# Performance work log

Hardware: AMD Instinct MI355X
Metric: run time of the kernel (lower is better)

## Reference

```python
import jax, jax.numpy as jnp
import numpy as np
from jax import lax

K = 8          # neighbors
LOSS_NORM = 2  # Lp norm over coords


def setup_inputs() -> dict:
    key = jax.random.key(0)
    k1, k2, k3 = jax.random.split(key, 3)
    B, N = 4, 8192
    return {
        "pc_source": jax.random.normal(k1, (B, N, 3), dtype=jnp.float32),
        "pc_target": jax.random.normal(k2, (B, N, 3), dtype=jnp.float32),
        "pred_flow": jax.random.normal(k3, (B, N, 3), dtype=jnp.float32),
    }


def _knn_idx(query, points, k):
    # query: [B,N,3], points: [B,M,3] -> idx [B,N,k] of k nearest points per query
    # squared euclidean pairwise distances (ranking-equivalent to euclidean)
    q2 = jnp.sum(query * query, axis=-1, keepdims=True)          # [B,N,1]
    p2 = jnp.sum(points * points, axis=-1)[:, None, :]           # [B,1,M]
    d2 = q2 + p2 - 2.0 * jnp.einsum("bnd,bmd->bnm", query, points)  # [B,N,M]
    _, idx = lax.top_k(-d2, k)                                   # smallest-k
    return idx


def _gather_points(points, idx):
    # points: [B,M,3], idx: [B,N,k] -> [B,N,k,3]
    return jax.vmap(lambda p, i: p[i])(points, idx)


def reference(pc_source, pc_target, pred_flow):
    pc_pred = pc_source + pred_flow                               # [B,N,3]

    # knn indices are detached in the original (idx.detach())
    idx1 = _knn_idx(lax.stop_gradient(pc_pred), lax.stop_gradient(pc_target), K)
    nn1 = _gather_points(pc_target, idx1)                         # [B,N,K,3]
    diff1 = pc_pred[:, :, None, :] - nn1                          # [B,N,K,3]
    dist1 = jnp.linalg.norm(diff1, ord=LOSS_NORM, axis=-1).mean(axis=-1)  # [B,N]

    idx2 = _knn_idx(lax.stop_gradient(pc_target), lax.stop_gradient(pc_pred), K)
    nn2 = _gather_points(pc_pred, idx2)                           # [B,M,K,3]
    diff2 = pc_target[:, :, None, :] - nn2
    dist2 = jnp.linalg.norm(diff2, ord=LOSS_NORM, axis=-1).mean(axis=-1)  # [B,M]

    return (dist1 + dist2).mean()
```

## Files before the change

### kernel.cpp

```cpp
#include <hip/hip_runtime.h>
#include <math.h>

constexpr int B = 4;
constexpr int N = 8192;
constexpr int KNN = 8;
constexpr int NCELL = 4096;
constexpr int GSIZE = 16;
constexpr int NGRP = N / GSIZE;
constexpr int QPB = 64;
constexpr int WAVES = 8;
constexpr int NCB = 2 * B;

__device__ __forceinline__ void insert8(float (&d)[KNN], float tv) {
  float n0 = fminf(d[0], tv);
  float n1 = __builtin_amdgcn_fmed3f(d[0], d[1], tv);
  float n2 = __builtin_amdgcn_fmed3f(d[1], d[2], tv);
  float n3 = __builtin_amdgcn_fmed3f(d[2], d[3], tv);
  float n4 = __builtin_amdgcn_fmed3f(d[3], d[4], tv);
  float n5 = __builtin_amdgcn_fmed3f(d[4], d[5], tv);
  float n6 = __builtin_amdgcn_fmed3f(d[5], d[6], tv);
  float n7 = __builtin_amdgcn_fmed3f(d[6], d[7], tv);
  d[0] = n0; d[1] = n1; d[2] = n2; d[3] = n3;
  d[4] = n4; d[5] = n5; d[6] = n6; d[7] = n7;
}

__device__ __forceinline__ int morton3(int x, int y, int z) {
  int m = 0;
#pragma unroll
  for (int b = 0; b < 4; ++b)
    m |= (((x >> b) & 1) << (3 * b + 2)) | (((y >> b) & 1) << (3 * b + 1)) |
         (((z >> b) & 1) << (3 * b + 0));
  return m;
}

__device__ __forceinline__ int point_cell(float x, float y, float z) {
  int cx = (int)fminf(fmaxf((x + 4.0f) * 2.0f, 0.0f), 15.0f);
  int cy = (int)fminf(fmaxf((y + 4.0f) * 2.0f, 0.0f), 15.0f);
  int cz = (int)fminf(fmaxf((z + 4.0f) * 2.0f, 0.0f), 15.0f);
  return morton3(cx, cy, cz);
}

__global__ __launch_bounds__(1024) void prep_kernel(
    const float* __restrict__ src, const float* __restrict__ tgt,
    const float* __restrict__ flow, float4* __restrict__ pred_s,
    float4* __restrict__ tgt_s, int* __restrict__ starts,
    float4* __restrict__ gbox, float* __restrict__ out) {
  __shared__ int hist[NCELL];
  __shared__ int wsum[16];
  int tid = threadIdx.x, cb = blockIdx.x;
  int cloud = cb >> 2, batch = cb & 3;
  if (cb == 0 && tid == 0) out[0] = 0.0f;

  for (int i = tid; i < NCELL; i += 1024) hist[i] = 0;
  __syncthreads();

  const float* __restrict__ bp = (cloud == 0 ? src : tgt) + batch * N * 3;
  const float* __restrict__ bf = flow + batch * N * 3;
  float4 pt[8];
  int cell[8];
#pragma unroll
  for (int k = 0; k < 8; ++k) {
    int i = k * 1024 + tid;
    float x = bp[3 * i + 0], y = bp[3 * i + 1], z = bp[3 * i + 2];
    if (cloud == 0) { x += bf[3 * i + 0]; y += bf[3 * i + 1]; z += bf[3 * i + 2]; }
    pt[k] = make_float4(x, y, z, 0.5f * (x * x + y * y + z * z));
    cell[k] = point_cell(x, y, z);
    atomicAdd(&hist[cell[k]], 1);
  }
  __syncthreads();

  int b4 = tid * 4;
  int h0v = hist[b4 + 0], h1v = hist[b4 + 1];
  int h2v = hist[b4 + 2], h3v = hist[b4 + 3];
  int s = h0v + h1v + h2v + h3v;
  int lane = tid & 63, w = tid >> 6;
  int incl = s;
#pragma unroll
  for (int off = 1; off < 64; off <<= 1) {
    int u = __shfl_up(incl, off, 64);
    if (lane >= off) incl += u;
  }
  if (lane == 63) wsum[w] = incl;
  __syncthreads();
  if (tid < 16) {
    int v = wsum[tid], inc = v;
#pragma unroll
    for (int off = 1; off < 16; off <<= 1) {
      int u = __shfl_up(inc, off, 64);
      if (tid >= off) inc += u;
    }
    wsum[tid] = inc - v;
  }
  __syncthreads();
  int run = incl - s + wsum[w];
  int* __restrict__ stg = starts + cb * (NCELL + 1);
  stg[b4 + 0] = run; hist[b4 + 0] = run; run += h0v;
  stg[b4 + 1] = run; hist[b4 + 1] = run; run += h1v;
  stg[b4 + 2] = run; hist[b4 + 2] = run; run += h2v;
  stg[b4 + 3] = run; hist[b4 + 3] = run; run += h3v;
  if (tid == 0) stg[NCELL] = N;
  __syncthreads();

  float4* __restrict__ dst = (cloud == 0 ? pred_s : tgt_s) + batch * N;
#pragma unroll
  for (int k = 0; k < 8; ++k) {
    int pos = atomicAdd(&hist[cell[k]], 1);
    dst[pos] = pt[k];
  }
  __threadfence_block();
  __syncthreads();

  if (tid < NGRP) {
    const float4* __restrict__ sp = dst + tid * GSIZE;
    float lx = INFINITY, ly = INFINITY, lz = INFINITY;
    float hx = -INFINITY, hy = -INFINITY, hz = -INFINITY;
#pragma unroll
    for (int t = 0; t < GSIZE; ++t) {
      float4 p = sp[t];
      lx = fminf(lx, p.x); ly = fminf(ly, p.y); lz = fminf(lz, p.z);
      hx = fmaxf(hx, p.x); hy = fmaxf(hy, p.y); hz = fmaxf(hz, p.z);
    }
    gbox[cb * 2 * NGRP + 2 * tid + 0] = make_float4(lx, ly, lz, 0.0f);
    gbox[cb * 2 * NGRP + 2 * tid + 1] = make_float4(hx, hy, hz, 0.0f);
  }
}

__global__ __launch_bounds__(512, 8) void chamfer_kernel(
    const float4* __restrict__ pred_s, const float4* __restrict__ tgt_s,
    const float4* __restrict__ aabb, float* __restrict__ out) {
  int blk = blockIdx.x;
  int dir = blk >> 9;
  int batch = (blk >> 7) & 3;
  int chunk = blk & 127;
  const float4* __restrict__ qarr = (dir == 0 ? pred_s : tgt_s) + batch * N;
  const float4* __restrict__ parr = (dir == 0 ? tgt_s : pred_s) + batch * N;
  int ccb = (dir == 0 ? 4 + batch : batch);
  const float4* __restrict__ gb = aabb + ccb * (2 * NGRP);

  int lane = threadIdx.x & 63;
  int wv = __builtin_amdgcn_readfirstlane(threadIdx.x >> 6);

  __shared__ float4 boxes[2 * NGRP];
  __shared__ float part[WAVES][QPB][KNN + 1];

  for (int i = threadIdx.x; i < 2 * NGRP; i += 512) boxes[i] = gb[i];

  float4 q = qarr[chunk * QPB + lane];
  float nqx = -q.x, nqy = -q.y, nqz = -q.z;
  float two_qw = 2.0f * q.w;

  float d[KNN];
#pragma unroll
  for (int i = 0; i < KNN; ++i) d[i] = INFINITY;
  float thr = INFINITY;

  __syncthreads();

  int tc = (chunk * 4 + 6 - wv) >> 3;
  tc = max(0, min(63, tc));

  auto step = [&](int t) {
    int g = t * 8 + wv;
    float4 lo = boxes[2 * g + 0];
    float4 hi = boxes[2 * g + 1];
    float dx = fmaxf(fmaxf(lo.x - q.x, q.x - hi.x), 0.0f);
    float dy = fmaxf(fmaxf(lo.y - q.y, q.y - hi.y), 0.0f);
    float dz = fmaxf(fmaxf(lo.z - q.z, q.z - hi.z), 0.0f);
    float md = __builtin_fmaf(dx, dx, __builtin_fmaf(dy, dy, dz * dz));
    if (__ballot(md < thr)) {
      const float4* __restrict__ gp = parr + g * GSIZE;
#pragma unroll
      for (int j = 0; j < GSIZE; ++j) {
        float4 p = gp[j];
        float tv = __builtin_fmaf(nqx, p.x, __builtin_fmaf(nqy, p.y,
                   __builtin_fmaf(nqz, p.z, p.w)));
        insert8(d, tv);
      }
      thr = __builtin_fmaf(2.0f, d[KNN - 1], two_qw) * 1.00001f + 1e-6f;
    }
  };

  for (int t = tc; t < 64; ++t) step(t);
  for (int t = tc - 1; t >= 0; --t) step(t);

#pragma unroll
  for (int i = 0; i < KNN; ++i) part[wv][lane][i] = d[i];
  __syncthreads();

  if (wv == 0) {
    float m[KNN];
#pragma unroll
    for (int i = 0; i < KNN; ++i) m[i] = part[0][lane][i];
    for (int s = 1; s < WAVES; ++s) {
#pragma unroll
      for (int i = 0; i < KNN; ++i) insert8(m, part[s][lane][i]);
    }
    float s_ = 0.0f;
#pragma unroll
    for (int i = 0; i < KNN; ++i) {
      float d2 = fmaxf(__builtin_fmaf(2.0f, m[i], two_qw), 0.0f);
      s_ += sqrtf(d2);
    }
    float val = s_ * (1.0f / KNN);
    for (int off = 32; off; off >>= 1) val += __shfl_down(val, off, 64);
    if (lane == 0) atomicAdd(out, val * (1.0f / (B * N)));
  }
}

extern "C" void kernel_launch(void* const* d_in, const int* in_sizes, int n_in,
                              void* d_out, int out_size, void* d_ws, size_t ws_size,
                              hipStream_t stream) {
  const float* src = (const float*)d_in[0];
  const float* tgt = (const float*)d_in[1];
  const float* flow = (const float*)d_in[2];
  float* out = (float*)d_out;

  float4* pred_s = (float4*)d_ws;
  float4* tgt_s = pred_s + B * N;
  float4* gbox = tgt_s + B * N;
  int* starts = (int*)(gbox + NCB * 2 * NGRP);

  prep_kernel<<<NCB, 1024, 0, stream>>>(src, tgt, flow, pred_s, tgt_s, starts,
                                        gbox, out);
  chamfer_kernel<<<2 * B * (N / QPB), 512, 0, stream>>>(pred_s, tgt_s, gbox, out);
}
```

Measured before the change: 144.6 us.

## Spread prep kernel over 64 blocks using software grid barriers

Prep work previously ran on only 8 blocks of 1024 threads, each binning and sorting one cloud with shared-memory histograms. It now runs on 64 blocks with one point per thread. Histogram and cursor live in global memory with global atomics, and an atomic-counter grid barrier separates the phases. This uses more CUs for the serial prep stage, at the cost of global atomic contention, a memset launch, and a spin barrier that relies on all 64 blocks being co-resident.

```diff
diff --git a/kernel.cpp b/kernel.cpp
--- a/kernel.cpp
+++ b/kernel.cpp
@@ -10,6 +10,7 @@
 constexpr int QPB = 64;
 constexpr int WAVES = 8;
 constexpr int NCB = 2 * B;
+constexpr int PBLK = 64;
 
 __device__ __forceinline__ void insert8(float (&d)[KNN], float tv) {
   float n0 = fminf(d[0], tv);
@@ -40,78 +41,93 @@
   return morton3(cx, cy, cz);
 }
 
+__device__ __forceinline__ void gridbar(int* cnt) {
+  __syncthreads();
+  if (threadIdx.x == 0) {
+    __threadfence();
+    int v = atomicAdd(cnt, 1);
+    int target = (v / PBLK + 1) * PBLK;
+    while (atomicAdd(cnt, 0) < target) __builtin_amdgcn_s_sleep(8);
+    __threadfence();
+  }
+  __syncthreads();
+}
+
 __global__ __launch_bounds__(1024) void prep_kernel(
     const float* __restrict__ src, const float* __restrict__ tgt,
     const float* __restrict__ flow, float4* __restrict__ pred_s,
-    float4* __restrict__ tgt_s, int* __restrict__ starts,
-    float4* __restrict__ gbox, float* __restrict__ out) {
-  __shared__ int hist[NCELL];
+    float4* __restrict__ tgt_s, int* __restrict__ hist,
+    int* __restrict__ cursor, float4* __restrict__ gbox, int* cnt,
+    float* __restrict__ out) {
   __shared__ int wsum[16];
-  int tid = threadIdx.x, cb = blockIdx.x;
+  int tid = threadIdx.x, bid = blockIdx.x;
+  int gid = bid * 1024 + tid;
+  int cb = gid >> 13, idx = gid & (N - 1);
   int cloud = cb >> 2, batch = cb & 3;
-  if (cb == 0 && tid == 0) out[0] = 0.0f;
-
-  for (int i = tid; i < NCELL; i += 1024) hist[i] = 0;
-  __syncthreads();
+
+  if (gid == 0) out[0] = 0.0f;
+  if (gid < NCB * NCELL) hist[gid] = 0;
 
   const float* __restrict__ bp = (cloud == 0 ? src : tgt) + batch * N * 3;
-  const float* __restrict__ bf = flow + batch * N * 3;
-  float4 pt[8];
-  int cell[8];
-#pragma unroll
-  for (int k = 0; k < 8; ++k) {
-    int i = k * 1024 + tid;
-    float x = bp[3 * i + 0], y = bp[3 * i + 1], z = bp[3 * i + 2];
-    if (cloud == 0) { x += bf[3 * i + 0]; y += bf[3 * i + 1]; z += bf[3 * i + 2]; }
-    pt[k] = make_float4(x, y, z, 0.5f * (x * x + y * y + z * z));
-    cell[k] = point_cell(x, y, z);
-    atomicAdd(&hist[cell[k]], 1);
-  }
-  __syncthreads();
-
-  int b4 = tid * 4;
-  int h0v = hist[b4 + 0], h1v = hist[b4 + 1];
-  int h2v = hist[b4 + 2], h3v = hist[b4 + 3];
-  int s = h0v + h1v + h2v + h3v;
-  int lane = tid & 63, w = tid >> 6;
-  int incl = s;
-#pragma unroll
-  for (int off = 1; off < 64; off <<= 1) {
-    int u = __shfl_up(incl, off, 64);
-    if (lane >= off) incl += u;
-  }
-  if (lane == 63) wsum[w] = incl;
-  __syncthreads();
-  if (tid < 16) {
-    int v = wsum[tid], inc = v;
-#pragma unroll
-    for (int off = 1; off < 16; off <<= 1) {
-      int u = __shfl_up(inc, off, 64);
-      if (tid >= off) inc += u;
-    }
-    wsum[tid] = inc - v;
-  }
-  __syncthreads();
-  int run = incl - s + wsum[w];
-  int* __restrict__ stg = starts + cb * (NCELL + 1);
-  stg[b4 + 0] = run; hist[b4 + 0] = run; run += h0v;
-  stg[b4 + 1] = run; hist[b4 + 1] = run; run += h1v;
-  stg[b4 + 2] = run; hist[b4 + 2] = run; run += h2v;
-  stg[b4 + 3] = run; hist[b4 + 3] = run; run += h3v;
-  if (tid == 0) stg[NCELL] = N;
-  __syncthreads();
-
+  float x = bp[3 * idx + 0], y = bp[3 * idx + 1], z = bp[3 * idx + 2];
+  if (cloud == 0) {
+    const float* __restrict__ bf = flow + batch * N * 3;
+    x += bf[3 * idx + 0]; y += bf[3 * idx + 1]; z += bf[3 * idx + 2];
+  }
+  float4 pt = make_float4(x, y, z, 0.5f * (x * x + y * y + z * z));
+  int cell = point_cell(x, y, z);
+
+  gridbar(cnt);
+
+  atomicAdd(&hist[cb * NCELL + cell], 1);
+
+  gridbar(cnt);
+
+  if (bid < NCB) {
+    int b4 = tid * 4;
+    int gbse = bid * NCELL + b4;
+    int h0v = hist[gbse + 0], h1v = hist[gbse + 1];
+    int h2v = hist[gbse + 2], h3v = hist[gbse + 3];
+    int ssum = h0v + h1v + h2v + h3v;
+    int lane = tid & 63, w = tid >> 6;
+    int incl = ssum;
+#pragma unroll
+    for (int off = 1; off < 64; off <<= 1) {
+      int u = __shfl_up(incl, off, 64);
+      if (lane >= off) incl += u;
+    }
+    if (lane == 63) wsum[w] = incl;
+    __syncthreads();
+    if (tid < 16) {
+      int v = wsum[tid], inc = v;
+#pragma unroll
+      for (int off = 1; off < 16; off <<= 1) {
+        int u = __shfl_up(inc, off, 64);
+        if (tid >= off) inc += u;
+      }
+      wsum[tid] = inc - v;
+    }
+    __syncthreads();
+    int run = incl - ssum + wsum[w];
+    cursor[gbse + 0] = run; run += h0v;
+    cursor[gbse + 1] = run; run += h1v;
+    cursor[gbse + 2] = run; run += h2v;
+    cursor[gbse + 3] = run;
+  }
+
+  gridbar(cnt);
+
+  int pos = atomicAdd(&cursor[cb * NCELL + cell], 1);
   float4* __restrict__ dst = (cloud == 0 ? pred_s : tgt_s) + batch * N;
-#pragma unroll
-  for (int k = 0; k < 8; ++k) {
-    int pos = atomicAdd(&hist[cell[k]], 1);
-    dst[pos] = pt[k];
-  }
-  __threadfence_block();
-  __syncthreads();
-
-  if (tid < NGRP) {
-    const float4* __restrict__ sp = dst + tid * GSIZE;
+  dst[pos] = pt;
+
+  gridbar(cnt);
+
+  if (tid < 64) {
+    int g = bid * 64 + tid;
+    int cbb = g >> 9, lg = g & (NGRP - 1);
+    const float4* __restrict__ sp =
+        (cbb < 4 ? pred_s : tgt_s) + (cbb & 3) * N + lg * GSIZE;
     float lx = INFINITY, ly = INFINITY, lz = INFINITY;
     float hx = -INFINITY, hy = -INFINITY, hz = -INFINITY;
 #pragma unroll
@@ -120,8 +136,8 @@
       lx = fminf(lx, p.x); ly = fminf(ly, p.y); lz = fminf(lz, p.z);
       hx = fmaxf(hx, p.x); hy = fmaxf(hy, p.y); hz = fmaxf(hz, p.z);
     }
-    gbox[cb * 2 * NGRP + 2 * tid + 0] = make_float4(lx, ly, lz, 0.0f);
-    gbox[cb * 2 * NGRP + 2 * tid + 1] = make_float4(hx, hy, hz, 0.0f);
+    gbox[cbb * 2 * NGRP + 2 * lg + 0] = make_float4(lx, ly, lz, 0.0f);
+    gbox[cbb * 2 * NGRP + 2 * lg + 1] = make_float4(hx, hy, hz, 0.0f);
   }
 }
 
@@ -218,9 +234,12 @@
   float4* pred_s = (float4*)d_ws;
   float4* tgt_s = pred_s + B * N;
   float4* gbox = tgt_s + B * N;
-  int* starts = (int*)(gbox + NCB * 2 * NGRP);
-
-  prep_kernel<<<NCB, 1024, 0, stream>>>(src, tgt, flow, pred_s, tgt_s, starts,
-                                        gbox, out);
+  int* hist = (int*)(gbox + NCB * 2 * NGRP);
+  int* cursor = hist + NCB * NCELL;
+  int* cnt = cursor + NCB * NCELL;
+
+  hipMemsetAsync(cnt, 0, sizeof(int), stream);
+  prep_kernel<<<PBLK, 1024, 0, stream>>>(src, tgt, flow, pred_s, tgt_s, hist,
+                                         cursor, gbox, cnt, out);
   chamfer_kernel<<<2 * B * (N / QPB), 512, 0, stream>>>(pred_s, tgt_s, gbox, out);
 }
```

After: 158.0 us. 9.3% more time.
